# Optimization experiments

Measured on AMD Instinct MI355X. Metric: run time of the kernel, lower is better.

Reference implementation:

```python
import jax, jax.numpy as jnp
import numpy as np

B, K, D, DICT, C = 2048, 32, 768, 24576, 64


def setup_inputs() -> dict:
    key = jax.random.key(0)
    ks = jax.random.split(key, 9)
    up_vals = jax.random.uniform(ks[0], (B, K), dtype=jnp.float32)
    up_decoder_w = jax.random.normal(ks[1], (D, DICT), dtype=jnp.float32) * 0.02
    down_encoder_w = jax.random.normal(ks[2], (DICT, D), dtype=jnp.float32) * 0.02
    up_encoder_w = jax.random.normal(ks[3], (DICT, D), dtype=jnp.float32) * 0.02
    b_dec = jax.random.normal(ks[4], (D,), dtype=jnp.float32) * 0.02
    up_indices = jax.random.randint(ks[5], (B, K), 0, DICT)
    down_indices = jax.random.randint(ks[6], (B, K), 0, DICT)
    conn = jax.random.randint(ks[7], (DICT, C), 0, DICT)
    drop = jax.random.uniform(ks[8], (DICT, C)) < 0.1
    connections = jnp.where(drop, -1, conn)
    return {
        "up_vals": up_vals,
        "up_decoder_w": up_decoder_w,
        "down_encoder_w": down_encoder_w,
        "up_encoder_w": up_encoder_w,
        "b_dec": b_dec,
        "up_indices": up_indices,
        "down_indices": down_indices,
        "connections": connections,
    }


def reference(up_vals, up_decoder_w, down_encoder_w, up_encoder_w, b_dec,
              up_indices, down_indices, connections):
    # allowed upstream features per active downstream feature: [B, k_down, C]
    allowed = connections[down_indices]
    valid = allowed != -1
    # match[b,i,c,j] = allowed[b,i,c] == up_indices[b,j] (and slot valid)
    match = (allowed[..., None] == up_indices[:, None, None, :]) & valid[..., None]
    # multiplicity of each (down i, up j) pair across the C slots: [B, k_down, k_up]
    mult = match.sum(axis=2).astype(up_vals.dtype)
    # gather active decoder/encoder vectors
    act_up = up_decoder_w.T[up_indices]          # [B, k_up, D]
    act_down = down_encoder_w[down_indices]      # [B, k_down, D]
    # virtual weights between active down and up features
    vw = jnp.einsum('bid,bjd->bij', act_down, act_up)  # [B, k_down, k_up]
    contributions = jnp.einsum('bij,bij->bi', vw, mult * up_vals[:, None, :])
    # bias contribution (note: indexed by up_indices, broadcast add as in source)
    b_dec_contrib = up_encoder_w @ b_dec         # [DICT]
    return contributions + b_dec_contrib[up_indices]
```

## Files before the change

### kernel.cpp

```cpp
#include <hip/hip_runtime.h>

#define B_    2048
#define K_    32
#define D_    768
#define DICT_ 24576
#define C_    64

__global__ void bdc_kernel(const float* __restrict__ up_enc,
                           const float* __restrict__ b_dec,
                           float* __restrict__ bdc) {
    int wave = threadIdx.x >> 6;
    int lane = threadIdx.x & 63;
    int row  = blockIdx.x * 4 + wave;
    const float4* rp = (const float4*)(up_enc + (size_t)row * D_);
    const float4* bp = (const float4*)b_dec;
    float acc = 0.f;
    #pragma unroll
    for (int i = 0; i < 3; ++i) {
        float4 a = rp[lane + 64 * i];
        float4 b = bp[lane + 64 * i];
        acc += a.x * b.x + a.y * b.y + a.z * b.z + a.w * b.w;
    }
    #pragma unroll
    for (int off = 32; off; off >>= 1) acc += __shfl_xor(acc, off);
    if (lane == 0) bdc[row] = acc;
}

__global__ void main_kernel(const float* __restrict__ up_vals,
                            const float* __restrict__ up_dec,
                            const float* __restrict__ down_enc,
                            const float* __restrict__ up_enc,
                            const float* __restrict__ b_dec,
                            const int*   __restrict__ up_idx,
                            const int*   __restrict__ down_idx,
                            const int*   __restrict__ conn,
                            const float* __restrict__ bdc,
                            float* __restrict__ out) {
    int wave = threadIdx.x >> 6;
    int lane = threadIdx.x & 63;
    int item = blockIdx.x * 4 + wave;
    int b    = item >> 5;

    int di = down_idx[item];
    int allowed = conn[(size_t)di * C_ + lane];
    bool valid = allowed >= 0;
    int   myup  = up_idx[b * K_ + (lane & 31)];
    float myval = up_vals[b * K_ + (lane & 31)];

    unsigned jm = 0u;
    #pragma unroll
    for (int j = 0; j < K_; ++j) {
        int tgt = __builtin_amdgcn_readlane(myup, j);
        jm |= (valid && (allowed == tgt)) ? (1u << j) : 0u;
    }

    float acc = 0.f;
    if (__ballot(jm != 0u)) {
        const float* drow = down_enc + (size_t)di * D_;
        #pragma unroll 1
        for (int j = 0; j < K_; ++j) {
            unsigned long long m = __ballot((jm >> j) & 1u);
            if (m != 0) {
                float w   = (float)__popcll(m) * __shfl(myval, j);
                int   tgt = __shfl(myup, j);
                const float* colp = up_dec + tgt;
                float partial = 0.f;
                #pragma unroll
                for (int ii = 0; ii < 12; ++ii) {
                    int d = lane + 64 * ii;
                    partial += drow[d] * colp[(size_t)d * DICT_];
                }
                acc += w * partial;
            }
        }
    }

    if (!bdc) {
        int ui = up_idx[item];
        const float4* rp = (const float4*)(up_enc + (size_t)ui * D_);
        const float4* bp = (const float4*)b_dec;
        #pragma unroll
        for (int ii = 0; ii < 3; ++ii) {
            float4 a  = rp[lane + 64 * ii];
            float4 bb = bp[lane + 64 * ii];
            acc += a.x * bb.x + a.y * bb.y + a.z * bb.z + a.w * bb.w;
        }
    }

    #pragma unroll
    for (int off = 32; off; off >>= 1) acc += __shfl_xor(acc, off);
    if (lane == 0) {
        float bias = bdc ? bdc[up_idx[item]] : 0.f;
        out[item] = acc + bias;
    }
}

extern "C" void kernel_launch(void* const* d_in, const int* in_sizes, int n_in,
                              void* d_out, int out_size, void* d_ws, size_t ws_size,
                              hipStream_t stream) {
    (void)in_sizes; (void)n_in; (void)out_size;
    const float* up_vals  = (const float*)d_in[0];
    const float* up_dec   = (const float*)d_in[1];
    const float* down_enc = (const float*)d_in[2];
    const float* up_enc   = (const float*)d_in[3];
    const float* b_dec    = (const float*)d_in[4];
    const int*   up_idx   = (const int*)d_in[5];
    const int*   down_idx = (const int*)d_in[6];
    const int*   conn     = (const int*)d_in[7];
    float* out = (float*)d_out;

    size_t bdc_bytes = (size_t)DICT_ * sizeof(float);
    float* bdc = (ws_size >= bdc_bytes) ? (float*)d_ws : nullptr;

    if (bdc) {
        bdc_kernel<<<DICT_ / 4, 256, 0, stream>>>(up_enc, b_dec, bdc);
    }
    main_kernel<<<(B_ * K_) / 4, 256, 0, stream>>>(up_vals, up_dec, down_enc,
                                                   up_enc, b_dec, up_idx,
                                                   down_idx, conn, bdc, out);
}
```

Before: 265.9 us.

## Transpose up_decoder_w into workspace so gathered columns are contiguous rows

Adds a tiled shared-memory transpose kernel that writes up_decoder_w transposed into the workspace, as a DICT x D matrix. The main kernel then reads each matched up-feature vector as a contiguous row using float4 loads. Before, it read a strided column with one cache line per element. This replaces scattered, uncoalesced gathers over roughly 98KB of cache lines per column with about 3KB of coalesced reads. In exchange, every call now reads and writes the full 75MB decoder matrix and needs a larger workspace. If the workspace is too small, the old strided path is used.

```diff
diff --git a/kernel.cpp b/kernel.cpp
--- a/kernel.cpp
+++ b/kernel.cpp
@@ -5,6 +5,35 @@
 #define D_    768
 #define DICT_ 24576
 #define C_    64
+
+__global__ __launch_bounds__(256) void transpose_kernel(const float* __restrict__ A,
+                                                        float* __restrict__ T) {
+    __shared__ float tile[64][65];
+    int fx = threadIdx.x & 15;
+    int fy = threadIdx.x >> 4;
+    int x0 = blockIdx.x * 64;
+    int y0 = blockIdx.y * 64;
+    #pragma unroll
+    for (int k = 0; k < 4; ++k) {
+        int d = y0 + fy + 16 * k;
+        float4 v = *(const float4*)(A + (size_t)d * DICT_ + x0 + 4 * fx);
+        tile[4 * fx + 0][fy + 16 * k] = v.x;
+        tile[4 * fx + 1][fy + 16 * k] = v.y;
+        tile[4 * fx + 2][fy + 16 * k] = v.z;
+        tile[4 * fx + 3][fy + 16 * k] = v.w;
+    }
+    __syncthreads();
+    #pragma unroll
+    for (int k = 0; k < 4; ++k) {
+        int row = fy + 16 * k;
+        float4 v;
+        v.x = tile[row][4 * fx + 0];
+        v.y = tile[row][4 * fx + 1];
+        v.z = tile[row][4 * fx + 2];
+        v.w = tile[row][4 * fx + 3];
+        *(float4*)(T + (size_t)(x0 + row) * D_ + y0 + 4 * fx) = v;
+    }
+}
 
 __global__ void bdc_kernel(const float* __restrict__ up_enc,
                            const float* __restrict__ b_dec,
@@ -34,6 +63,7 @@
                             const int*   __restrict__ up_idx,
                             const int*   __restrict__ down_idx,
                             const int*   __restrict__ conn,
+                            const float* __restrict__ T,
                             const float* __restrict__ bdc,
                             float* __restrict__ out) {
     int wave = threadIdx.x >> 6;
@@ -63,12 +93,23 @@
             if (m != 0) {
                 float w   = (float)__popcll(m) * __shfl(myval, j);
                 int   tgt = __shfl(myup, j);
-                const float* colp = up_dec + tgt;
                 float partial = 0.f;
-                #pragma unroll
-                for (int ii = 0; ii < 12; ++ii) {
-                    int d = lane + 64 * ii;
-                    partial += drow[d] * colp[(size_t)d * DICT_];
+                if (T) {
+                    const float4* cp = (const float4*)(T + (size_t)tgt * D_);
+                    const float4* dp = (const float4*)drow;
+                    #pragma unroll
+                    for (int ii = 0; ii < 3; ++ii) {
+                        float4 c = cp[lane + 64 * ii];
+                        float4 d = dp[lane + 64 * ii];
+                        partial += c.x * d.x + c.y * d.y + c.z * d.z + c.w * d.w;
+                    }
+                } else {
+                    const float* colp = up_dec + tgt;
+                    #pragma unroll
+                    for (int ii = 0; ii < 12; ++ii) {
+                        int d = lane + 64 * ii;
+                        partial += drow[d] * colp[(size_t)d * DICT_];
+                    }
                 }
                 acc += w * partial;
             }
@@ -110,12 +151,18 @@
     float* out = (float*)d_out;
 
     size_t bdc_bytes = (size_t)DICT_ * sizeof(float);
+    size_t T_bytes   = (size_t)DICT_ * D_ * sizeof(float);
     float* bdc = (ws_size >= bdc_bytes) ? (float*)d_ws : nullptr;
+    float* T   = (ws_size >= bdc_bytes + T_bytes) ? (float*)d_ws + DICT_ : nullptr;
 
+    if (T) {
+        dim3 grid(DICT_ / 64, D_ / 64);
+        transpose_kernel<<<grid, 256, 0, stream>>>(up_dec, T);
+    }
     if (bdc) {
         bdc_kernel<<<DICT_ / 4, 256, 0, stream>>>(up_enc, b_dec, bdc);
     }
-    main_kernel<<<(B_ * K_) / 4, 256, 0, stream>>>(up_vals, up_dec, down_enc,
-                                                   up_enc, b_dec, up_idx,
-                                                   down_idx, conn, bdc, out);
+    main_kernel<<<(B_ * K_) / 4, 256, 0, stream>>>(up_vals, up_dec, down_enc, up_enc,
+                                                   b_dec, up_idx, down_idx, conn,
+                                                   T, bdc, out);
 }
```

After: 256.9 us. 1.03x faster.

## Compact matching pairs and compute dots over coalesced decoder column tiles

Applied to the files above, without the earlier changes.

A scan kernel now writes the bias into the output and appends each matching (down item, up index, weight) pair to a global list using an atomic counter. A second kernel tiles up_decoder_w into 16x512 chunks held in shared memory, and each block filters the list for pairs whose column falls in its chunk. Those pairs are dotted against a 16-element slice of the down-encoder row and accumulated into the output with atomics. This replaces the per-pair strided column gather (one cache line per element) with coalesced tile loads. In exchange it streams the whole decoder matrix, accumulates the sum nondeterministically, and silently drops pairs if a chunk holds more than 512 or the list overflows its capacity.

```diff
diff --git a/kernel.cpp b/kernel.cpp
--- a/kernel.cpp
+++ b/kernel.cpp
@@ -6,9 +6,22 @@
 #define DICT_ 24576
 #define C_    64
 
+#define PAIR_CAP (1 << 18)
+#define CCHUNK   512
+#define DCHUNK   16
+#define NCC      (DICT_ / CCHUNK)
+#define NDC      (D_ / DCHUNK)
+
+#define BDC_F (PAIR_CAP * 4)
+#define CNT_F (BDC_F + DICT_)
+#define T_F   (CNT_F + 1)
+#define WS_FLOATS (T_F + PAIR_CAP)
+
 __global__ void bdc_kernel(const float* __restrict__ up_enc,
                            const float* __restrict__ b_dec,
-                           float* __restrict__ bdc) {
+                           float* __restrict__ bdc,
+                           int* __restrict__ cnt) {
+    if (blockIdx.x == 0 && threadIdx.x == 0) cnt[0] = 0;
     int wave = threadIdx.x >> 6;
     int lane = threadIdx.x & 63;
     int row  = blockIdx.x * 4 + wave;
@@ -26,16 +39,116 @@
     if (lane == 0) bdc[row] = acc;
 }
 
-__global__ void main_kernel(const float* __restrict__ up_vals,
-                            const float* __restrict__ up_dec,
-                            const float* __restrict__ down_enc,
-                            const float* __restrict__ up_enc,
-                            const float* __restrict__ b_dec,
+__global__ void scan_kernel(const float* __restrict__ up_vals,
+                            const float* __restrict__ bdc,
                             const int*   __restrict__ up_idx,
                             const int*   __restrict__ down_idx,
                             const int*   __restrict__ conn,
-                            const float* __restrict__ bdc,
+                            int*  __restrict__ cnt,
+                            int*  __restrict__ tArr,
+                            int4* __restrict__ recArr,
                             float* __restrict__ out) {
+    int wave = threadIdx.x >> 6;
+    int lane = threadIdx.x & 63;
+    int item = blockIdx.x * 4 + wave;
+    int b    = item >> 5;
+
+    int di = down_idx[item];
+    int allowed = conn[(size_t)di * C_ + lane];
+    bool valid = allowed >= 0;
+    int   myup  = up_idx[b * K_ + (lane & 31)];
+    float myval = up_vals[b * K_ + (lane & 31)];
+
+    if (lane == 0) out[item] = bdc[up_idx[item]];
+
+    unsigned jm = 0u;
+    #pragma unroll
+    for (int j = 0; j < K_; ++j) {
+        int tgt = __builtin_amdgcn_readlane(myup, j);
+        jm |= (valid && (allowed == tgt)) ? (1u << j) : 0u;
+    }
+
+    if (__ballot(jm != 0u)) {
+        #pragma unroll 1
+        for (int j = 0; j < K_; ++j) {
+            unsigned long long m = __ballot((jm >> j) & 1u);
+            if (m != 0) {
+                int   t = __shfl(myup, j);
+                float w = (float)__popcll(m) * __shfl(myval, j);
+                if (lane == 0) {
+                    int pos = atomicAdd(cnt, 1);
+                    if (pos < PAIR_CAP) {
+                        tArr[pos]   = t;
+                        recArr[pos] = make_int4(item, di, __float_as_int(w), 0);
+                    }
+                }
+            }
+        }
+    }
+}
+
+__global__ __launch_bounds__(256) void pair_dot_kernel(const float* __restrict__ A,
+                                                       const float* __restrict__ down_enc,
+                                                       const int*  __restrict__ cnt,
+                                                       const int*  __restrict__ tArr,
+                                                       const int4* __restrict__ recArr,
+                                                       float* __restrict__ out) {
+    __shared__ float tile[DCHUNK * CCHUNK];
+    __shared__ int   lidx[512];
+    __shared__ int   lcnt;
+    int tid = threadIdx.x;
+    if (tid == 0) lcnt = 0;
+    __syncthreads();
+
+    int cc = blockIdx.x, dc = blockIdx.y;
+    int c0 = cc * CCHUNK, d0 = dc * DCHUNK;
+
+    int n = *cnt; if (n > PAIR_CAP) n = PAIR_CAP;
+    for (int i = tid; i < n; i += 256) {
+        if ((tArr[i] >> 9) == cc) {
+            int s = atomicAdd(&lcnt, 1);
+            if (s < 512) lidx[s] = i;
+        }
+    }
+    __syncthreads();
+    int ln = lcnt < 512 ? lcnt : 512;
+    if (ln == 0) return;
+
+    #pragma unroll
+    for (int k = 0; k < 8; ++k) {
+        int l  = tid + 256 * k;
+        int r  = l >> 7, fi = l & 127;
+        ((float4*)tile)[l] = *(const float4*)(A + (size_t)(d0 + r) * DICT_ + c0 + 4 * fi);
+    }
+    __syncthreads();
+
+    for (int i = tid; i < ln; i += 256) {
+        int idx = lidx[i];
+        int4 rec = recArr[idx];
+        int t = tArr[idx] - c0;
+        const float4* dp = (const float4*)(down_enc + (size_t)rec.y * D_ + d0);
+        float acc = 0.f;
+        #pragma unroll
+        for (int q = 0; q < 4; ++q) {
+            float4 dv = dp[q];
+            acc += dv.x * tile[(4 * q + 0) * CCHUNK + t]
+                 + dv.y * tile[(4 * q + 1) * CCHUNK + t]
+                 + dv.z * tile[(4 * q + 2) * CCHUNK + t]
+                 + dv.w * tile[(4 * q + 3) * CCHUNK + t];
+        }
+        atomicAdd(out + rec.x, __int_as_float(rec.z) * acc);
+    }
+}
+
+__global__ void main_fallback(const float* __restrict__ up_vals,
+                              const float* __restrict__ up_dec,
+                              const float* __restrict__ down_enc,
+                              const float* __restrict__ up_enc,
+                              const float* __restrict__ b_dec,
+                              const int*   __restrict__ up_idx,
+                              const int*   __restrict__ down_idx,
+                              const int*   __restrict__ conn,
+                              float* __restrict__ out) {
     int wave = threadIdx.x >> 6;
     int lane = threadIdx.x & 63;
     int item = blockIdx.x * 4 + wave;
@@ -75,7 +188,7 @@
         }
     }
 
-    if (!bdc) {
+    {
         int ui = up_idx[item];
         const float4* rp = (const float4*)(up_enc + (size_t)ui * D_);
         const float4* bp = (const float4*)b_dec;
@@ -89,10 +202,7 @@
 
     #pragma unroll
     for (int off = 32; off; off >>= 1) acc += __shfl_xor(acc, off);
-    if (lane == 0) {
-        float bias = bdc ? bdc[up_idx[item]] : 0.f;
-        out[item] = acc + bias;
-    }
+    if (lane == 0) out[item] = acc;
 }
 
 extern "C" void kernel_launch(void* const* d_in, const int* in_sizes, int n_in,
@@ -109,13 +219,22 @@
     const int*   conn     = (const int*)d_in[7];
     float* out = (float*)d_out;
 
-    size_t bdc_bytes = (size_t)DICT_ * sizeof(float);
-    float* bdc = (ws_size >= bdc_bytes) ? (float*)d_ws : nullptr;
-
-    if (bdc) {
-        bdc_kernel<<<DICT_ / 4, 256, 0, stream>>>(up_enc, b_dec, bdc);
-    }
-    main_kernel<<<(B_ * K_) / 4, 256, 0, stream>>>(up_vals, up_dec, down_enc,
-                                                   up_enc, b_dec, up_idx,
-                                                   down_idx, conn, bdc, out);
-}
+    if (ws_size < (size_t)WS_FLOATS * sizeof(float)) {
+        main_fallback<<<(B_ * K_) / 4, 256, 0, stream>>>(up_vals, up_dec, down_enc,
+                                                         up_enc, b_dec, up_idx,
+                                                         down_idx, conn, out);
+        return;
+    }
+
+    float* ws     = (float*)d_ws;
+    int4*  recArr = (int4*)ws;
+    float* bdc    = ws + BDC_F;
+    int*   cnt    = (int*)(ws + CNT_F);
+    int*   tArr   = (int*)(ws + T_F);
+
+    bdc_kernel<<<DICT_ / 4, 256, 0, stream>>>(up_enc, b_dec, bdc, cnt);
+    scan_kernel<<<(B_ * K_) / 4, 256, 0, stream>>>(up_vals, bdc, up_idx, down_idx,
+                                                   conn, cnt, tArr, recArr, out);
+    pair_dot_kernel<<<dim3(NCC, NDC), 256, 0, stream>>>(up_dec, down_enc, cnt,
+                                                        tArr, recArr, out);
+}
```

Result: slower. 293.6 us (+10.4%).
